# Kernel tuning notes

Hardware: AMD Instinct MI355X
Metric: run time of the kernel (lower is better)

Reference implementation:

```python
import jax, jax.numpy as jnp
import numpy as np


def setup_inputs() -> dict:
    key = jax.random.key(0)
    ks = jax.random.split(key, 5)
    B, T, I, H, O = 256, 2048, 256, 256, 16
    x = jax.random.normal(ks[0], (B, T, I), dtype=jnp.float32)
    W_ih = jax.random.normal(ks[1], (I, H), dtype=jnp.float32) * 0.05
    W_hh = jax.random.normal(ks[2], (H, H), dtype=jnp.float32) * 0.05
    b_h = jnp.zeros((H,), dtype=jnp.float32)
    fc_w = jax.random.normal(ks[3], (O, H), dtype=jnp.float32) * 0.05
    fc_b = jnp.zeros((O,), dtype=jnp.float32)
    return {"x": x, "W_ih": W_ih, "W_hh": W_hh, "b_h": b_h, "fc_w": fc_w, "fc_b": fc_b}


def reference(x, W_ih, W_hh, b_h, fc_w, fc_b):
    # x: [B, T, I]. Precompute input projections for all timesteps in one GEMM,
    # then scan the strictly sequential hidden-state recurrence.
    B, T, I = x.shape
    H = W_hh.shape[0]
    xp = jnp.einsum('bti,ih->tbh', x, W_ih) + b_h  # [T, B, H]

    def step(h, xt):
        h = jnp.tanh(xt + h @ W_hh)
        return h, None

    h0 = jnp.zeros((B, H), dtype=x.dtype)
    h_final, _ = jax.lax.scan(step, h0, xp)
    return h_final @ fc_w.T + fc_b  # [B, O]
```

## Files before the change

kernel.cpp:

```cpp
#include <hip/hip_runtime.h>
#include <hip/hip_bf16.h>


typedef _Float16 f16;
typedef _Float16 h8_t __attribute__((ext_vector_type(8)));
typedef _Float16 h2_t __attribute__((ext_vector_type(2)));
typedef float    f4_t __attribute__((ext_vector_type(4)));

__device__ __forceinline__ float fdot2u(unsigned w, unsigned h, float c) {
  return __builtin_amdgcn_fdot2(__builtin_bit_cast(h2_t, w),
                                __builtin_bit_cast(h2_t, h), c, false);
}
__device__ __forceinline__ unsigned pkrtz(float a, float b) {
  return __builtin_bit_cast(unsigned, __builtin_amdgcn_cvt_pkrtz(a, b));
}

__global__ __launch_bounds__(256) void prep_kernel(const float* __restrict__ Wih,
                                                   const float* __restrict__ Whh,
                                                   uint4* __restrict__ Wfrag,
                                                   uint4* __restrict__ Wc2) {
  int idx = blockIdx.x * 256 + threadIdx.x;
  int e = idx & 8191;
  int gi = e >> 8;
  int lg = e & 255;
  int w = lg >> 6, l = lg & 63;
  unsigned r[4];
  if (idx < 8192) {
    int nt = gi >> 3, ks = gi & 7;
    int n = w * 64 + nt * 16 + (l & 15);
    int k0 = ks * 32 + (l >> 4) * 8;
#pragma unroll
    for (int c = 0; c < 4; ++c)
      r[c] = pkrtz(Wih[(k0 + 2 * c) * 256 + n], Wih[(k0 + 2 * c + 1) * 256 + n]);
    Wfrag[gi * 256 + lg] = make_uint4(r[0], r[1], r[2], r[3]);
  } else {
    int oi = gi >> 3, q2 = gi & 7;
    int j = l + 64 * oi;
    int kb = 64 * w + 8 * q2;
#pragma unroll
    for (int c = 0; c < 4; ++c)
      r[c] = pkrtz(Whh[(kb + 2 * c) * 256 + j], Whh[(kb + 2 * c + 1) * 256 + j]);
    Wc2[gi * 256 + lg] = make_uint4(r[0], r[1], r[2], r[3]);
  }
}

__global__ __launch_bounds__(256, 2) void gemm_kernel(const float* __restrict__ x,
                                                      const uint4* __restrict__ Wfrag,
                                                      f16* __restrict__ xp,
                                                      int t0, int CT, int tpc) {
  __shared__ f16 As[64][264];
  int tid = threadIdx.x;
  int wave = tid >> 6, l = tid & 63, l15 = l & 15, q = l >> 4;

  uint4 bf[4][8];
#pragma unroll
  for (int nt = 0; nt < 4; ++nt)
#pragma unroll
    for (int ks = 0; ks < 8; ++ks)
      bf[nt][ks] = Wfrag[(nt * 8 + ks) * 256 + tid];

  int blk = blockIdx.x;
  int b = blk / tpc, tt = blk - b * tpc;
  int tl0 = tt * 64;

  const uint4* xsrc = (const uint4*)(x + ((size_t)b * 2048 + t0 + tl0) * 256);
#pragma unroll
  for (int i = 0; i < 16; ++i) {
    int fi = i * 256 + tid;
    float4 f = __builtin_bit_cast(float4, xsrc[fi]);
    int row = fi >> 6;
    int k = (fi & 63) * 4;
    uint2 pv; pv.x = pkrtz(f.x, f.y); pv.y = pkrtz(f.z, f.w);
    *(uint2*)&As[row][k] = pv;
  }
  __syncthreads();

  f4_t acc[4][4];
#pragma unroll
  for (int mt = 0; mt < 4; ++mt)
#pragma unroll
    for (int nt = 0; nt < 4; ++nt) acc[mt][nt] = (f4_t){0.f, 0.f, 0.f, 0.f};

  for (int mt = 0; mt < 4; ++mt) {
    uint4 af[8];
#pragma unroll
    for (int ks = 0; ks < 8; ++ks)
      af[ks] = *(const uint4*)&As[mt * 16 + l15][ks * 32 + q * 8];
#pragma unroll
    for (int ks = 0; ks < 8; ++ks) {
      h8_t a = __builtin_bit_cast(h8_t, af[ks]);
#pragma unroll
      for (int nt = 0; nt < 4; ++nt)
        acc[mt][nt] = __builtin_amdgcn_mfma_f32_16x16x32_f16(
            a, __builtin_bit_cast(h8_t, bf[nt][ks]), acc[mt][nt], 0, 0, 0);
    }
  }

  f16* xpo = xp + (size_t)b * CT * 256;
#pragma unroll
  for (int mt = 0; mt < 4; ++mt)
#pragma unroll
    for (int nt = 0; nt < 4; ++nt) {
      int n = wave * 64 + nt * 16 + l15;
#pragma unroll
      for (int r = 0; r < 4; ++r)
        xpo[(size_t)(tl0 + mt * 16 + q * 4 + r) * 256 + n] = (f16)acc[mt][nt][r];
    }
}

__global__ __launch_bounds__(256, 1) void rnn_kernel(const f16* __restrict__ xp,
                                                     const uint4* __restrict__ Wc2,
                                                     const float* __restrict__ b_h,
                                                     const float* __restrict__ fc_w,
                                                     const float* __restrict__ fc_b,
                                                     float* __restrict__ hstate,
                                                     float* __restrict__ out,
                                                     int t0, int CT) {
  __shared__ f16 hbuf[2][256];
  __shared__ float prt[4][256];
  __shared__ float hf[256];
  __shared__ float prt2[16][16];

  int b = blockIdx.x, tid = threadIdx.x;
  int w = tid >> 6, l = tid & 63;

  uint4 wv[32];
#pragma unroll
  for (int g = 0; g < 32; ++g) wv[g] = Wc2[g * 256 + tid];

  float hcur = (t0 == 0) ? 0.0f : hstate[b * 256 + tid];
  hbuf[0][tid] = (f16)hcur;
  float bhv = b_h[tid];

  const f16* xpb = xp + (size_t)b * CT * 256 + tid;
  float xv = (float)xpb[0];
  float xn = (float)xpb[256];
  __syncthreads();

  for (int tt = 0; tt < CT; ++tt) {
    int pf = (tt + 2 < CT) ? tt + 2 : CT - 1;
    f16 xf = xpb[(size_t)pf * 256];

    const uint4* hb = (const uint4*)&hbuf[tt & 1][w * 64];
    uint4 hh[8];
#pragma unroll
    for (int q2 = 0; q2 < 8; ++q2) hh[q2] = hb[q2];

    float s[4];
#pragma unroll
    for (int oi = 0; oi < 4; ++oi) {
      float a0 = 0.f, a1 = 0.f;
#pragma unroll
      for (int q2 = 0; q2 < 8; ++q2) {
        uint4 wq = wv[oi * 8 + q2];
        a0 = fdot2u(wq.x, hh[q2].x, a0);
        a1 = fdot2u(wq.y, hh[q2].y, a1);
        a0 = fdot2u(wq.z, hh[q2].z, a0);
        a1 = fdot2u(wq.w, hh[q2].w, a1);
      }
      s[oi] = a0 + a1;
    }
#pragma unroll
    for (int oi = 0; oi < 4; ++oi) prt[w][l + 64 * oi] = s[oi];
    __syncthreads();

    float z = prt[0][tid] + prt[1][tid] + prt[2][tid] + prt[3][tid] + xv + bhv;
    float e = __expf(2.0f * z);
    hcur = 1.0f - 2.0f * __builtin_amdgcn_rcpf(e + 1.0f);
    hbuf[(tt + 1) & 1][tid] = (f16)hcur;
    xv = xn;
    xn = (float)xf;
    __syncthreads();
  }

  hstate[b * 256 + tid] = hcur;

  if (t0 + CT == 2048) {
    hf[tid] = hcur;
    __syncthreads();
    int o = tid >> 4, s2 = tid & 15;
    const float* fw = fc_w + o * 256 + s2 * 16;
    float p = 0.f;
#pragma unroll
    for (int i = 0; i < 16; ++i) p += hf[s2 * 16 + i] * fw[i];
    prt2[o][s2] = p;
    __syncthreads();
    if (tid < 16) {
      float r = fc_b[tid];
#pragma unroll
      for (int s3 = 0; s3 < 16; ++s3) r += prt2[tid][s3];
      out[b * 16 + tid] = r;
    }
  }
}

extern "C" void kernel_launch(void* const* d_in, const int* in_sizes, int n_in,
                              void* d_out, int out_size, void* d_ws, size_t ws_size,
                              hipStream_t stream) {
  const float* x   = (const float*)d_in[0];
  const float* Wih = (const float*)d_in[1];
  const float* Whh = (const float*)d_in[2];
  const float* bh  = (const float*)d_in[3];
  const float* fcw = (const float*)d_in[4];
  const float* fcb = (const float*)d_in[5];
  float* out = (float*)d_out;

  char* ws = (char*)d_ws;
  uint4* Wfrag  = (uint4*)ws;
  uint4* Wc2    = (uint4*)(ws + (128 << 10));
  float* hstate = (float*)(ws + (256 << 10));
  f16*   xpb    = (f16*)(ws + (512 << 10));

  size_t avail = (ws_size > (size_t)(512 << 10)) ? ws_size - (size_t)(512 << 10) : 0;
  int CT = 2048;
  while (CT > 64 && (size_t)CT * 131072 > avail) CT >>= 1;
  int tpc = CT >> 6;

  prep_kernel<<<64, 256, 0, stream>>>(Wih, Whh, Wfrag, Wc2);
  for (int t0 = 0; t0 < 2048; t0 += CT) {
    gemm_kernel<<<256 * tpc, 256, 0, stream>>>(x, Wfrag, xpb, t0, CT, tpc);
    rnn_kernel<<<256, 256, 0, stream>>>(xpb, Wc2, bh, fcw, fcb, hstate, out, t0, CT);
  }
}
```

Baseline: 1.973 ms.

## Compute each hidden unit's full dot product per thread, dropping the partial-sum reduction

The W_hh fragment layout changes so each thread holds the whole K=256 column for its own output unit. Each thread then reads the entire h vector from LDS (broadcast) and accumulates its full dot product into 8 independent accumulators, which removes the prt partial-sum buffer and one of the two barriers per step. The loop is also unrolled by 4 with a 4-deep x prefetch, and a raw s_barrier with an explicit lgkmcnt wait replaces __syncthreads. In exchange every thread performs 8x more LDS reads of h per step and there are longer dependent chains, although the reads are broadcasts.

```diff
diff --git a/kernel.cpp b/kernel.cpp
--- a/kernel.cpp
+++ b/kernel.cpp
@@ -34,9 +34,8 @@
       r[c] = pkrtz(Wih[(k0 + 2 * c) * 256 + n], Wih[(k0 + 2 * c + 1) * 256 + n]);
     Wfrag[gi * 256 + lg] = make_uint4(r[0], r[1], r[2], r[3]);
   } else {
-    int oi = gi >> 3, q2 = gi & 7;
-    int j = l + 64 * oi;
-    int kb = 64 * w + 8 * q2;
+    int j = lg;
+    int kb = gi * 8;
 #pragma unroll
     for (int c = 0; c < 4; ++c)
       r[c] = pkrtz(Whh[(kb + 2 * c) * 256 + j], Whh[(kb + 2 * c + 1) * 256 + j]);
@@ -116,13 +115,11 @@
                                                      float* __restrict__ hstate,
                                                      float* __restrict__ out,
                                                      int t0, int CT) {
-  __shared__ f16 hbuf[2][256];
-  __shared__ float prt[4][256];
+  __shared__ __align__(16) f16 hbuf[2][256];
   __shared__ float hf[256];
   __shared__ float prt2[16][16];
 
   int b = blockIdx.x, tid = threadIdx.x;
-  int w = tid >> 6, l = tid & 63;
 
   uint4 wv[32];
 #pragma unroll
@@ -133,45 +130,53 @@
   float bhv = b_h[tid];
 
   const f16* xpb = xp + (size_t)b * CT * 256 + tid;
-  float xv = (float)xpb[0];
-  float xn = (float)xpb[256];
+  float xv = (float)xpb[0] + bhv;
+  f16 n0, n1, n2, n3;
+  n1 = xpb[256];
+  n2 = xpb[512];
+  n3 = xpb[768];
   __syncthreads();
 
-  for (int tt = 0; tt < CT; ++tt) {
-    int pf = (tt + 2 < CT) ? tt + 2 : CT - 1;
-    f16 xf = xpb[(size_t)pf * 256];
-
-    const uint4* hb = (const uint4*)&hbuf[tt & 1][w * 64];
-    uint4 hh[8];
-#pragma unroll
-    for (int q2 = 0; q2 < 8; ++q2) hh[q2] = hb[q2];
-
-    float s[4];
-#pragma unroll
-    for (int oi = 0; oi < 4; ++oi) {
-      float a0 = 0.f, a1 = 0.f;
-#pragma unroll
-      for (int q2 = 0; q2 < 8; ++q2) {
-        uint4 wq = wv[oi * 8 + q2];
-        a0 = fdot2u(wq.x, hh[q2].x, a0);
-        a1 = fdot2u(wq.y, hh[q2].y, a1);
-        a0 = fdot2u(wq.z, hh[q2].z, a0);
-        a1 = fdot2u(wq.w, hh[q2].w, a1);
-      }
-      s[oi] = a0 + a1;
-    }
-#pragma unroll
-    for (int oi = 0; oi < 4; ++oi) prt[w][l + 64 * oi] = s[oi];
-    __syncthreads();
-
-    float z = prt[0][tid] + prt[1][tid] + prt[2][tid] + prt[3][tid] + xv + bhv;
-    float e = __expf(2.0f * z);
-    hcur = 1.0f - 2.0f * __builtin_amdgcn_rcpf(e + 1.0f);
-    hbuf[(tt + 1) & 1][tid] = (f16)hcur;
-    xv = xn;
-    xn = (float)xf;
-    __syncthreads();
-  }
+#define RNN_STEP(T, PAR, NLOAD, NUSE)                                       \
+  {                                                                         \
+    int pf = (T) + 4;                                                       \
+    if (pf > CT - 1) pf = CT - 1;                                           \
+    NLOAD = xpb[(size_t)pf * 256];                                          \
+    const uint4* hb = (const uint4*)&hbuf[PAR][0];                          \
+    float a0 = 0.f, a1 = 0.f, a2 = 0.f, a3 = 0.f;                           \
+    float a4 = 0.f, a5 = 0.f, a6 = 0.f, a7 = 0.f;                           \
+    _Pragma("unroll") for (int g8 = 0; g8 < 4; ++g8) {                      \
+      uint4 hh[8];                                                          \
+      _Pragma("unroll") for (int u = 0; u < 8; ++u) hh[u] = hb[g8 * 8 + u]; \
+      _Pragma("unroll") for (int u = 0; u < 8; u += 2) {                    \
+        uint4 w0 = wv[g8 * 8 + u], w1 = wv[g8 * 8 + u + 1];                 \
+        a0 = fdot2u(w0.x, hh[u].x, a0);                                     \
+        a1 = fdot2u(w0.y, hh[u].y, a1);                                     \
+        a2 = fdot2u(w0.z, hh[u].z, a2);                                     \
+        a3 = fdot2u(w0.w, hh[u].w, a3);                                     \
+        a4 = fdot2u(w1.x, hh[u + 1].x, a4);                                 \
+        a5 = fdot2u(w1.y, hh[u + 1].y, a5);                                 \
+        a6 = fdot2u(w1.z, hh[u + 1].z, a6);                                 \
+        a7 = fdot2u(w1.w, hh[u + 1].w, a7);                                 \
+      }                                                                     \
+    }                                                                       \
+    float z = ((a0 + a4) + (a1 + a5)) + (((a2 + a6) + (a3 + a7)) + xv);     \
+    float e = __expf(2.0f * z);                                             \
+    hcur = 1.0f - 2.0f * __builtin_amdgcn_rcpf(e + 1.0f);                   \
+    hbuf[(PAR) ^ 1][tid] = (f16)hcur;                                       \
+    xv = (float)(NUSE) + bhv;                                               \
+    asm volatile("s_waitcnt lgkmcnt(0)" ::: "memory");                      \
+    __builtin_amdgcn_s_barrier();                                           \
+    __builtin_amdgcn_sched_barrier(0);                                      \
+  }
+
+  for (int tt = 0; tt < CT; tt += 4) {
+    RNN_STEP(tt + 0, 0, n0, n1)
+    RNN_STEP(tt + 1, 1, n1, n2)
+    RNN_STEP(tt + 2, 0, n2, n3)
+    RNN_STEP(tt + 3, 1, n3, n0)
+  }
+#undef RNN_STEP
 
   hstate[b * 256 + tid] = hcur;
 
```

Result: faster. 1.914 ms (-3.0%).
